# Performance work log

Hardware: AMD Instinct MI355X
Metric: run time of the kernel (lower is better)

Reference implementation:

```python
import jax, jax.numpy as jnp
import numpy as np

B, N, F_DIM = 64, 4096, 64
K_SLOTS, D, N_ITERS = 8, 64, 3
EPS = 1e-8
LN_EPS = 1e-5  # torch LayerNorm default


def layernorm(x, g, b):
    mu = jnp.mean(x, axis=-1, keepdims=True)
    var = jnp.mean(jnp.square(x - mu), axis=-1, keepdims=True)
    return (x - mu) * jax.lax.rsqrt(var + LN_EPS) * g + b


def gru_cell(x, h, w_ih, w_hh, b_ih, b_hh):
    # torch.nn.GRUCell semantics; weights are [3D, D] with gate order r, z, n
    gi = x @ w_ih.T + b_ih
    gh = h @ w_hh.T + b_hh
    i_r, i_z, i_n = jnp.split(gi, 3, axis=-1)
    h_r, h_z, h_n = jnp.split(gh, 3, axis=-1)
    r = jax.nn.sigmoid(i_r + h_r)
    z = jax.nn.sigmoid(i_z + h_z)
    n = jnp.tanh(i_n + r * h_n)
    return (1.0 - z) * n + z * h


def setup_inputs() -> dict:
    key = jax.random.key(0)
    ks = jax.random.split(key, 16)
    f32 = jnp.float32
    s = 0.05  # small init scale for weights
    return {
        "inputs": jax.random.normal(ks[0], (B, N, F_DIM), f32),
        "slots_noise": jax.random.normal(ks[1], (B, K_SLOTS, D), f32),
        "slots_mu": jax.random.normal(ks[2], (1, 1, D), f32) * s,
        "slots_log_sigma": jax.random.normal(ks[3], (1, 1, D), f32) * s,
        "Wq": jax.random.normal(ks[4], (D, D), f32) * s,
        "Wk": jax.random.normal(ks[5], (D, F_DIM), f32) * s,
        "Wv": jax.random.normal(ks[6], (D, F_DIM), f32) * s,
        "gru_w_ih": jax.random.normal(ks[7], (3 * D, D), f32) * s,
        "gru_w_hh": jax.random.normal(ks[8], (3 * D, D), f32) * s,
        "gru_b_ih": jnp.zeros((3 * D,), f32),
        "gru_b_hh": jnp.zeros((3 * D,), f32),
        "mlp_w1": jax.random.normal(ks[9], (2 * D, D), f32) * s,
        "mlp_b1": jnp.zeros((2 * D,), f32),
        "mlp_w2": jax.random.normal(ks[10], (D, 2 * D), f32) * s,
        "mlp_b2": jnp.zeros((D,), f32),
        "ln_in_g": jnp.ones((F_DIM,), f32), "ln_in_b": jnp.zeros((F_DIM,), f32),
        "ln_slots_g": jnp.ones((D,), f32), "ln_slots_b": jnp.zeros((D,), f32),
        "ln_mlp_g": jnp.ones((D,), f32), "ln_mlp_b": jnp.zeros((D,), f32),
    }


def reference(inputs, slots_noise, slots_mu, slots_log_sigma, Wq, Wk, Wv,
              gru_w_ih, gru_w_hh, gru_b_ih, gru_b_hh,
              mlp_w1, mlp_b1, mlp_w2, mlp_b2,
              ln_in_g, ln_in_b, ln_slots_g, ln_slots_b, ln_mlp_g, ln_mlp_b):
    x = layernorm(inputs, ln_in_g, ln_in_b)          # [B, N, F]
    k = jnp.einsum('bnf,df->bnd', x, Wk)             # [B, N, D]
    v = jnp.einsum('bnf,df->bnd', x, Wv)             # [B, N, D]

    slots = slots_mu + jnp.exp(slots_log_sigma) * slots_noise  # [B, K, D]
    scale = D ** -0.5

    for _ in range(N_ITERS):
        slots_prev = slots
        s_n = layernorm(slots, ln_slots_g, ln_slots_b)
        q = jnp.einsum('bkd,ed->bke', s_n, Wq)                  # [B, K, D]
        attn_logits = jnp.einsum('bnd,bkd->bnk', k, q) * scale  # [B, N, K]
        attn = jax.nn.softmax(attn_logits, axis=-1) + EPS       # softmax over slots
        attn = attn / jnp.sum(attn, axis=1, keepdims=True)      # renormalize over N
        updates = jnp.einsum('bnk,bnd->bkd', attn, v)           # [B, K, D]
        slots = gru_cell(updates.reshape(-1, D), slots_prev.reshape(-1, D),
                         gru_w_ih, gru_w_hh, gru_b_ih, gru_b_hh).reshape(B, K_SLOTS, D)
        h = layernorm(slots, ln_mlp_g, ln_mlp_b)
        h = jax.nn.relu(h @ mlp_w1.T + mlp_b1) @ mlp_w2.T + mlp_b2
        slots = slots + h
    return slots
```

## Files before the change

kernel.cpp:

```cpp
#include <hip/hip_runtime.h>
#include <math.h>

#define NN 4096
#define LN_EPS 1e-5f
#define EPS 1e-8f

typedef unsigned short ushortT;
typedef unsigned int uintT;
typedef __attribute__((ext_vector_type(8))) short short8;
typedef __attribute__((ext_vector_type(4))) float f32x4;
typedef __attribute__((ext_vector_type(4))) unsigned short us4;

#define OFF_XN    0L
#define OFF_QT    33554432L
#define OFF_ACC   33587200L
#define OFF_COL   33619968L
#define OFF_SLOTS 33620480L
#define OFF_WIHT  33653248L
#define OFF_WHHT  33665536L
#define OFF_W1T   33677824L
#define OFF_W2T   33686016L
#define OFF_WQT   33694208L
#define OFF_WVT   33698304L
#define OFF_CNT   33702400L

__device__ __forceinline__ float wredsum(float v) {
#pragma unroll
  for (int off = 32; off > 0; off >>= 1) v += __shfl_xor(v, off);
  return v;
}

__device__ __forceinline__ ushortT f2bf(float f) {
  uintT b = __float_as_uint(f);
  b += 0x7fff + ((b >> 16) & 1);
  return (ushortT)(b >> 16);
}

__global__ __launch_bounds__(256) void k_prep(
    const float* __restrict__ w_ih, const float* __restrict__ w_hh,
    const float* __restrict__ w1, const float* __restrict__ w2,
    const float* __restrict__ Wq, const float* __restrict__ Wv,
    float* __restrict__ wihT, float* __restrict__ whhT,
    float* __restrict__ w1T, float* __restrict__ w2T, float* __restrict__ wqT,
    float* __restrict__ wvT, uintT* __restrict__ cnt)
{
  int idx = blockIdx.x * 256 + threadIdx.x;
  if (idx < 12288) {
    int j = idx >> 6, f = idx & 63;
    wihT[f * 192 + j] = w_ih[idx];
  } else if (idx < 24576) {
    int i = idx - 12288; int j = i >> 6, f = i & 63;
    whhT[f * 192 + j] = w_hh[i];
  } else if (idx < 32768) {
    int i = idx - 24576; int j = i >> 6, f = i & 63;
    w1T[f * 128 + j] = w1[i];
  } else if (idx < 40960) {
    int i = idx - 32768; int d = i >> 7, j = i & 127;
    w2T[j * 64 + d] = w2[i];
  } else if (idx < 45056) {
    int i = idx - 40960; int e = i >> 6, d = i & 63;
    wqT[d * 64 + e] = Wq[i];
  } else if (idx < 49152) {
    int i = idx - 45056; int d = i >> 6, f = i & 63;
    wvT[f * 64 + d] = Wv[i];
  } else if (idx < 49216) {
    cnt[idx - 49152] = 0u;
  }
}

__global__ __launch_bounds__(256) void k_ln_init(
    const float* __restrict__ inp,
    const float* __restrict__ g, const float* __restrict__ bbv,
    ushortT* __restrict__ xnG,
    const float* __restrict__ noise, const float* __restrict__ smu,
    const float* __restrict__ slsig, const float* __restrict__ wqT,
    const float* __restrict__ Wk,
    const float* __restrict__ g_sl, const float* __restrict__ b_sl,
    float* __restrict__ slots, ushortT* __restrict__ qF,
    float* __restrict__ acc, float* __restrict__ colsum)
{
  __shared__ __align__(16) ushortT xnF[4096];
  const int tid = threadIdx.x;
  const int lane = tid & 63;
  const int wave = tid >> 6;

  if (blockIdx.x >= 4096) {
    const int bi = blockIdx.x - 4096;
    const int row = bi * 4 + wave;
    const int b = row >> 3, ks = row & 7;
    float* SI = (float*)&xnF[0];
    float* Sw = SI + (wave << 9);

    float s0 = fmaf(expf(slsig[lane]), noise[row * 64 + lane], smu[lane]);
    slots[row * 64 + lane] = s0;
    acc[row * 64 + lane] = 0.f;
    if (lane == 0) colsum[row] = 0.f;

    float mu = wredsum(s0) * (1.f / 64.f);
    float dx = s0 - mu;
    float var = wredsum(dx * dx) * (1.f / 64.f);
    float sn = dx * rsqrtf(var + LN_EPS) * g_sl[lane] + b_sl[lane];
    Sw[lane] = sn;
    float qe = 0.f;
#pragma unroll 16
    for (int d = 0; d < 64; ++d) qe = fmaf(Sw[d], wqT[d * 64 + lane], qe);
    Sw[64 + lane] = qe;
    float qp = 0.f;
#pragma unroll 16
    for (int e = 0; e < 64; ++e) qp = fmaf(Sw[64 + e], Wk[e * 64 + lane], qp);
    const int kb = lane >> 5, lrow = (lane & 31) >> 3, j = lane & 7;
    qF[((((b * 2 + kb) << 6) + (lrow << 4) + ks) << 3) + j] = f2bf(qp * 0.125f);
    qF[((((b * 2 + kb) << 6) + (lrow << 4) + 8 + ks) << 3) + j] = 0;
    return;
  }

  const int l15 = lane & 15, q = lane >> 4;
  const int tile = blockIdx.x;
  const int b = tile >> 6;
  const int c = tile & 63;
  const int n0 = c << 6;
  const float* rowbase = inp + (((long)b * NN + n0) << 6);
  const float4 g4 = *(const float4*)&g[l15 << 2];
  const float4 b4 = *(const float4*)&bbv[l15 << 2];

#pragma unroll
  for (int i = 0; i < 4; ++i) {
    const int row = (wave << 4) + (i << 2) + q;
    float4 x = *(const float4*)&rowbase[(row << 6) + (l15 << 2)];
    float s = x.x + x.y + x.z + x.w;
    s += __shfl_xor(s, 1); s += __shfl_xor(s, 2);
    s += __shfl_xor(s, 4); s += __shfl_xor(s, 8);
    const float mu = s * (1.f / 64.f);
    float4 dx = {x.x - mu, x.y - mu, x.z - mu, x.w - mu};
    float ss = dx.x * dx.x + dx.y * dx.y + dx.z * dx.z + dx.w * dx.w;
    ss += __shfl_xor(ss, 1); ss += __shfl_xor(ss, 2);
    ss += __shfl_xor(ss, 4); ss += __shfl_xor(ss, 8);
    const float rs = rsqrtf(ss * (1.f / 64.f) + LN_EPS);
    us4 p = {f2bf(dx.x * rs * g4.x + b4.x), f2bf(dx.y * rs * g4.y + b4.y),
             f2bf(dx.z * rs * g4.z + b4.z), f2bf(dx.w * rs * g4.w + b4.w)};
    *(us4*)&xnF[((((wave << 1) + (l15 >> 3)) << 6) + (((l15 & 7) >> 1) << 4)
                 + (row & 15)) * 8 + ((l15 & 1) << 2)] = p;
  }
  __syncthreads();

  ushortT* dst = xnG + ((long)(b * 64 + c) << 12);
  short8 v0 = *(const short8*)&xnF[tid << 4];
  short8 v1 = *(const short8*)&xnF[(tid << 4) + 8];
  *(short8*)&dst[tid << 4] = v0;
  *(short8*)&dst[(tid << 4) + 8] = v1;
}

__global__ __launch_bounds__(256, 2) void k_attn(
    const ushortT* __restrict__ xnG,
    ushortT* __restrict__ qF,
    float* __restrict__ acc, float* __restrict__ colsum,
    uintT* __restrict__ cnt, float* __restrict__ slots,
    const float* __restrict__ wihT, const float* __restrict__ whhT,
    const float* __restrict__ w1T, const float* __restrict__ w2T,
    const float* __restrict__ wqT, const float* __restrict__ Wk,
    const float* __restrict__ wvT,
    const float* __restrict__ b_ih, const float* __restrict__ b_hh,
    const float* __restrict__ mb1, const float* __restrict__ mb2,
    const float* __restrict__ g_ml, const float* __restrict__ b_ml,
    const float* __restrict__ g_sl, const float* __restrict__ b_sl,
    float* __restrict__ dout)
{
  __shared__ __align__(16) ushortT XW[4][4096];
  __shared__ int lastFlag;
  const int tid = threadIdx.x;
  const int lane = tid & 63;
  const int wave = tid >> 6;
  const int l15 = lane & 15, q = lane >> 4;
  const int b = blockIdx.x >> 3;
  const int e = blockIdx.x & 7;

  ushortT* xT = &XW[wave][0];

  const ushortT* pc0 = xnG + ((long)(b * 64 + (e << 3) + wave) << 12);
  const ushortT* pc1 = pc0 + (4L << 12);

  short8 kA0[4][2], kA1[4][2];
#pragma unroll
  for (int mt = 0; mt < 4; ++mt)
#pragma unroll
    for (int kb = 0; kb < 2; ++kb) {
      kA0[mt][kb] = *(const short8*)&pc0[((mt * 2 + kb) * 64 + lane) << 3];
      kA1[mt][kb] = *(const short8*)&pc1[((mt * 2 + kb) * 64 + lane) << 3];
    }
  short8 qB[2];
#pragma unroll
  for (int kb = 0; kb < 2; ++kb)
    qB[kb] = *(const short8*)&qF[(((b * 2 + kb) << 6) + lane) << 3];

  f32x4 accP[4];
#pragma unroll
  for (int nt = 0; nt < 4; ++nt) accP[nt] = (f32x4){0.f, 0.f, 0.f, 0.f};
  float csum = 0.f;

  auto do_chunk = [&](const short8 (&kA)[4][2]) {
    f32x4 accL[4];
#pragma unroll
    for (int mt = 0; mt < 4; ++mt) {
      accL[mt] = (f32x4){0.f, 0.f, 0.f, 0.f};
      accL[mt] = __builtin_amdgcn_mfma_f32_16x16x32_bf16(kA[mt][0], qB[0], accL[mt], 0, 0, 0);
      accL[mt] = __builtin_amdgcn_mfma_f32_16x16x32_bf16(kA[mt][1], qB[1], accL[mt], 0, 0, 0);
    }

    {
      const int h = ((lane >> 5) << 2) | (((lane & 15) >> 3) << 1) | ((lane >> 4) & 1);
      const int jp = lane & 7;
      const int lpA = (((lane >> 4) & 1) << 3) + (((lane & 15) >> 3) << 4);
#pragma unroll
      for (int mt = 0; mt < 4; ++mt)
#pragma unroll
        for (int kb = 0; kb < 2; ++kb) {
          const int fb = (kb * 4 + ((lane >> 5) << 1) + (mt >> 1)) << 9;
          const int lm = lpA + ((mt & 1) << 5);
          const ushortT* src = (const ushortT*)&kA[mt][kb];
#pragma unroll
          for (int j = 0; j < 8; ++j)
            xT[fb + (((lm + j) ^ h) << 3) + jp] = src[j];
        }
    }
    short8 vB[4][2];
#pragma unroll
    for (int nt = 0; nt < 4; ++nt)
#pragma unroll
      for (int ks = 0; ks < 2; ++ks) {
        const int frag = nt * 2 + ks;
        const int hr = ((nt & 1) << 2) | (((lane >> 4) & 1) << 1) | ((lane >> 3) & 1);
        vB[nt][ks] = *(const short8*)&xT[(frag << 9) + ((lane ^ hr) << 3)];
      }

    ushortT* attnF = &XW[wave][0];
#pragma unroll
    for (int mt = 0; mt < 4; ++mt) {
      float av[4];
#pragma unroll
      for (int r = 0; r < 4; ++r) {
        float lv = accL[mt][r];
        float mx = lv;
        mx = fmaxf(mx, __shfl_xor(mx, 1));
        mx = fmaxf(mx, __shfl_xor(mx, 2));
        mx = fmaxf(mx, __shfl_xor(mx, 4));
        float ev = __expf(lv - mx);
        float sv = ev;
        sv += __shfl_xor(sv, 1); sv += __shfl_xor(sv, 2); sv += __shfl_xor(sv, 4);
        float a = ev * (1.f / sv) + EPS;
        av[r] = a;
        csum += a;
      }
      us4 p = {f2bf(av[0]), f2bf(av[1]), f2bf(av[2]), f2bf(av[3])};
      *(us4*)&attnF[((((mt >> 1) << 6) + (((mt & 1) * 2 + (q >> 1)) << 4)
                      + l15) << 3) + ((q & 1) << 2)] = p;
    }

    short8 pA0 = *(const short8*)&attnF[(0 * 64 + lane) << 3];
    short8 pA1 = *(const short8*)&attnF[(1 * 64 + lane) << 3];

#pragma unroll
    for (int nt = 0; nt < 4; ++nt) {
      accP[nt] = __builtin_amdgcn_mfma_f32_16x16x32_bf16(pA0, vB[nt][0], accP[nt], 0, 0, 0);
      accP[nt] = __builtin_amdgcn_mfma_f32_16x16x32_bf16(pA1, vB[nt][1], accP[nt], 0, 0, 0);
    }
  };

  do_chunk(kA0);
  do_chunk(kA1);

  csum += __shfl_xor(csum, 16);
  csum += __shfl_xor(csum, 32);

  float* accLw = (float*)&XW[wave][1024];
  float* colLw = (float*)&XW[wave][2048];
  if (q < 2) {
#pragma unroll
    for (int nt = 0; nt < 4; ++nt)
#pragma unroll
      for (int r = 0; r < 4; ++r)
        accLw[(q * 4 + r) * 64 + nt * 16 + l15] = accP[nt][r];
  }
  if (q == 0 && l15 < 8) colLw[l15] = csum;
  __syncthreads();

#pragma unroll
  for (int r = 0; r < 2; ++r) {
    const int o = tid + r * 256;
    const int kk = o >> 6, d = o & 63;
    float s = *((float*)&XW[0][1024] + kk * 64 + d)
            + *((float*)&XW[1][1024] + kk * 64 + d)
            + *((float*)&XW[2][1024] + kk * 64 + d)
            + *((float*)&XW[3][1024] + kk * 64 + d);
    atomicAdd(&acc[(b * 8 + kk) * 64 + d], s);
  }
  if (tid < 8) {
    float s = *((float*)&XW[0][2048] + tid) + *((float*)&XW[1][2048] + tid)
            + *((float*)&XW[2][2048] + tid) + *((float*)&XW[3][2048] + tid);
    atomicAdd(&colsum[b * 8 + tid], s);
  }

  __syncthreads();
  if (tid == 0) lastFlag = (atomicAdd(&cnt[b], 1u) == 7u);
  __syncthreads();
  if (!lastFlag) return;

  const int ks0 = wave, ks1 = wave + 4;
  const int row0 = b * 8 + ks0, row1 = b * 8 + ks1;

  float csv0 = 0.f, csv1 = 0.f;
  if (lane == 0) {
    csv0 = atomicAdd(&colsum[row0], 0.f);
    csv1 = atomicAdd(&colsum[row1], 0.f);
  }
  csv0 = __shfl(csv0, 0); csv1 = __shfl(csv1, 0);
  const float t0 = atomicAdd(&acc[row0 * 64 + lane], 0.f) / csv0;
  const float t1 = atomicAdd(&acc[row1 * 64 + lane], 0.f) / csv1;
  const float h0 = slots[row0 * 64 + lane];
  const float h1 = slots[row1 * 64 + lane];

  float* S = (float*)&XW[wave][0];

  S[256 + lane] = t0; S[320 + lane] = t1;
  float u0 = 0.f, u1 = 0.f;
#pragma unroll 4
  for (int f = 0; f < 64; ++f) {
    const float wv = wvT[f * 64 + lane];
    u0 = fmaf(S[256 + f], wv, u0);
    u1 = fmaf(S[320 + f], wv, u1);
  }

  S[lane] = u0; S[64 + lane] = u1; S[128 + lane] = h0; S[192 + lane] = h1;

  float gir0 = b_ih[lane], giz0 = b_ih[64 + lane], gin0 = b_ih[128 + lane];
  float ghr0 = b_hh[lane], ghz0 = b_hh[64 + lane], ghn0 = b_hh[128 + lane];
  float gir1 = gir0, giz1 = giz0, gin1 = gin0;
  float ghr1 = ghr0, ghz1 = ghz0, ghn1 = ghn0;
#pragma unroll 4
  for (int f = 0; f < 64; ++f) {
    const float wr = wihT[f * 192 + lane], wz = wihT[f * 192 + 64 + lane],
                wn = wihT[f * 192 + 128 + lane];
    const float vr = whhT[f * 192 + lane], vz = whhT[f * 192 + 64 + lane],
                vn = whhT[f * 192 + 128 + lane];
    const float a0 = S[f], a1 = S[64 + f], c0 = S[128 + f], c1 = S[192 + f];
    gir0 = fmaf(a0, wr, gir0); gir1 = fmaf(a1, wr, gir1);
    giz0 = fmaf(a0, wz, giz0); giz1 = fmaf(a1, wz, giz1);
    gin0 = fmaf(a0, wn, gin0); gin1 = fmaf(a1, wn, gin1);
    ghr0 = fmaf(c0, vr, ghr0); ghr1 = fmaf(c1, vr, ghr1);
    ghz0 = fmaf(c0, vz, ghz0); ghz1 = fmaf(c1, vz, ghz1);
    ghn0 = fmaf(c0, vn, ghn0); ghn1 = fmaf(c1, vn, ghn1);
  }
  const float r0 = 1.f / (1.f + expf(-(gir0 + ghr0)));
  const float z0 = 1.f / (1.f + expf(-(giz0 + ghz0)));
  const float n0 = tanhf(fmaf(r0, ghn0, gin0));
  const float hn0 = (1.f - z0) * n0 + z0 * h0;
  const float r1 = 1.f / (1.f + expf(-(gir1 + ghr1)));
  const float z1 = 1.f / (1.f + expf(-(giz1 + ghz1)));
  const float n1 = tanhf(fmaf(r1, ghn1, gin1));
  const float hn1 = (1.f - z1) * n1 + z1 * h1;

  float mu0 = wredsum(hn0) * (1.f / 64.f);
  float dx0 = hn0 - mu0;
  float va0 = wredsum(dx0 * dx0) * (1.f / 64.f);
  const float ln0 = dx0 * rsqrtf(va0 + LN_EPS) * g_ml[lane] + b_ml[lane];
  float mu1 = wredsum(hn1) * (1.f / 64.f);
  float dx1 = hn1 - mu1;
  float va1 = wredsum(dx1 * dx1) * (1.f / 64.f);
  const float ln1 = dx1 * rsqrtf(va1 + LN_EPS) * g_ml[lane] + b_ml[lane];
  S[256 + lane] = ln0; S[320 + lane] = ln1;

  float h1a0 = mb1[lane], h1b0 = mb1[64 + lane];
  float h1a1 = h1a0, h1b1 = h1b0;
#pragma unroll 4
  for (int f = 0; f < 64; ++f) {
    const float wa = w1T[f * 128 + lane], wb = w1T[f * 128 + 64 + lane];
    const float l0 = S[256 + f], l1 = S[320 + f];
    h1a0 = fmaf(l0, wa, h1a0); h1a1 = fmaf(l1, wa, h1a1);
    h1b0 = fmaf(l0, wb, h1b0); h1b1 = fmaf(l1, wb, h1b1);
  }
  h1a0 = fmaxf(h1a0, 0.f); h1b0 = fmaxf(h1b0, 0.f);
  h1a1 = fmaxf(h1a1, 0.f); h1b1 = fmaxf(h1b1, 0.f);
  S[lane] = h1a0; S[64 + lane] = h1b0;
  S[128 + lane] = h1a1; S[192 + lane] = h1b1;

  float o0 = mb2[lane], o1 = mb2[lane];
#pragma unroll 4
  for (int j = 0; j < 128; ++j) {
    const float w2v = w2T[j * 64 + lane];
    o0 = fmaf(S[j], w2v, o0);
    o1 = fmaf(S[128 + j], w2v, o1);
  }
  const float sn0 = hn0 + o0;
  const float sn1 = hn1 + o1;
  slots[row0 * 64 + lane] = sn0;
  slots[row1 * 64 + lane] = sn1;
  if (dout) {
    dout[row0 * 64 + lane] = sn0;
    dout[row1 * 64 + lane] = sn1;
  }

  float m20 = wredsum(sn0) * (1.f / 64.f);
  float d20 = sn0 - m20;
  float v20 = wredsum(d20 * d20) * (1.f / 64.f);
  const float sq0 = d20 * rsqrtf(v20 + LN_EPS) * g_sl[lane] + b_sl[lane];
  float m21 = wredsum(sn1) * (1.f / 64.f);
  float d21 = sn1 - m21;
  float v21 = wredsum(d21 * d21) * (1.f / 64.f);
  const float sq1 = d21 * rsqrtf(v21 + LN_EPS) * g_sl[lane] + b_sl[lane];
  S[256 + lane] = sq0; S[320 + lane] = sq1;
  float qe0 = 0.f, qe1 = 0.f;
#pragma unroll 8
  for (int d = 0; d < 64; ++d) {
    const float wq = wqT[d * 64 + lane];
    qe0 = fmaf(S[256 + d], wq, qe0);
    qe1 = fmaf(S[320 + d], wq, qe1);
  }
  S[384 + lane] = qe0; S[448 + lane] = qe1;
  float qp0 = 0.f, qp1 = 0.f;
#pragma unroll 8
  for (int e2 = 0; e2 < 64; ++e2) {
    const float wk = Wk[e2 * 64 + lane];
    qp0 = fmaf(S[384 + e2], wk, qp0);
    qp1 = fmaf(S[448 + e2], wk, qp1);
  }
  const int kb = lane >> 5, lrow = (lane & 31) >> 3, jj = lane & 7;
  qF[((((b * 2 + kb) << 6) + (lrow << 4) + ks0) << 3) + jj] = f2bf(qp0 * 0.125f);
  qF[((((b * 2 + kb) << 6) + (lrow << 4) + ks1) << 3) + jj] = f2bf(qp1 * 0.125f);

  acc[row0 * 64 + lane] = 0.f;
  acc[row1 * 64 + lane] = 0.f;
  if (lane == 0) { colsum[row0] = 0.f; colsum[row1] = 0.f; }
  if (tid == 0) cnt[b] = 0u;
}

extern "C" void kernel_launch(void* const* d_in, const int* in_sizes, int n_in,
                              void* d_out, int out_size, void* d_ws, size_t ws_size,
                              hipStream_t stream) {
  const float* inp   = (const float*)d_in[0];
  const float* noise = (const float*)d_in[1];
  const float* smu   = (const float*)d_in[2];
  const float* slsig = (const float*)d_in[3];
  const float* Wq    = (const float*)d_in[4];
  const float* Wk    = (const float*)d_in[5];
  const float* Wv    = (const float*)d_in[6];
  const float* w_ih  = (const float*)d_in[7];
  const float* w_hh  = (const float*)d_in[8];
  const float* b_ih  = (const float*)d_in[9];
  const float* b_hh  = (const float*)d_in[10];
  const float* w1    = (const float*)d_in[11];
  const float* b1    = (const float*)d_in[12];
  const float* w2    = (const float*)d_in[13];
  const float* b2    = (const float*)d_in[14];
  const float* g_in  = (const float*)d_in[15];
  const float* bi_in = (const float*)d_in[16];
  const float* g_sl  = (const float*)d_in[17];
  const float* bi_sl = (const float*)d_in[18];
  const float* g_ml  = (const float*)d_in[19];
  const float* bi_ml = (const float*)d_in[20];

  float* ws      = (float*)d_ws;
  ushortT* xnG   = (ushortT*)(ws + OFF_XN);
  ushortT* qF    = (ushortT*)(ws + OFF_QT);
  float* ac      = ws + OFF_ACC;
  float* cs      = ws + OFF_COL;
  float* sl      = ws + OFF_SLOTS;
  float* wihT    = ws + OFF_WIHT;
  float* whhT    = ws + OFF_WHHT;
  float* w1T     = ws + OFF_W1T;
  float* w2T     = ws + OFF_W2T;
  float* wqT     = ws + OFF_WQT;
  float* wvT     = ws + OFF_WVT;
  uintT* cnt     = (uintT*)(ws + OFF_CNT);

  k_prep<<<193, 256, 0, stream>>>(w_ih, w_hh, w1, w2, Wq, Wv,
                                  wihT, whhT, w1T, w2T, wqT, wvT, cnt);
  k_ln_init<<<4224, 256, 0, stream>>>(inp, g_in, bi_in, xnG,
                                      noise, smu, slsig, wqT, Wk, g_sl, bi_sl,
                                      sl, qF, ac, cs);
  for (int it = 0; it < 3; ++it) {
    k_attn<<<512, 256, 0, stream>>>(xnG, qF, ac, cs, cnt, sl,
                                    wihT, whhT, w1T, w2T, wqT, Wk, wvT,
                                    b_ih, b_hh, b1, b2, g_ml, bi_ml, g_sl, bi_sl,
                                    it == 2 ? (float*)d_out : nullptr);
  }
}
```

Before: 255.7 us.

## Fuse three attention iterations into one persistent kernel with per-batch ready flags

Replaces the three k_attn launches with a single launch. Each block keeps its bf16 K/V fragments in registers across all iterations and spin-waits on a per-batch ready counter that the last-arriving block bumps after it writes the new queries. The accumulators and counters are triple-buffered per iteration so nothing has to be reset between rounds, and the query handoff now goes through packed uint atomics. This removes two kernel launches and the repeated reload of the normalized inputs. It depends on all 512 blocks being co-resident (two per CU); if they are not, the spin-wait can deadlock.

```diff
diff --git a/kernel.cpp b/kernel.cpp
--- a/kernel.cpp
+++ b/kernel.cpp
@@ -12,17 +12,18 @@
 typedef __attribute__((ext_vector_type(4))) unsigned short us4;
 
 #define OFF_XN    0L
-#define OFF_QT    33554432L
-#define OFF_ACC   33587200L
-#define OFF_COL   33619968L
-#define OFF_SLOTS 33620480L
-#define OFF_WIHT  33653248L
-#define OFF_WHHT  33665536L
-#define OFF_W1T   33677824L
-#define OFF_W2T   33686016L
-#define OFF_WQT   33694208L
-#define OFF_WVT   33698304L
-#define OFF_CNT   33702400L
+#define OFF_QU    8388608L
+#define OFF_ACC   8421376L
+#define OFF_COL   8519680L
+#define OFF_SLOTS 8521216L
+#define OFF_WIHT  8553984L
+#define OFF_WHHT  8566272L
+#define OFF_W1T   8578560L
+#define OFF_W2T   8586752L
+#define OFF_WQT   8594944L
+#define OFF_WVT   8599040L
+#define OFF_CNT   8603136L
+#define OFF_RDY   8603328L
 
 __device__ __forceinline__ float wredsum(float v) {
 #pragma unroll
@@ -34,6 +35,10 @@
   uintT b = __float_as_uint(f);
   b += 0x7fff + ((b >> 16) & 1);
   return (ushortT)(b >> 16);
+}
+
+__device__ __forceinline__ uintT pack2bf(float lo, float hi) {
+  return (uintT)f2bf(lo) | ((uintT)f2bf(hi) << 16);
 }
 
 __global__ __launch_bounds__(256) void k_prep(
@@ -42,7 +47,7 @@
     const float* __restrict__ Wq, const float* __restrict__ Wv,
     float* __restrict__ wihT, float* __restrict__ whhT,
     float* __restrict__ w1T, float* __restrict__ w2T, float* __restrict__ wqT,
-    float* __restrict__ wvT, uintT* __restrict__ cnt)
+    float* __restrict__ wvT, uintT* __restrict__ cnt, uintT* __restrict__ ready)
 {
   int idx = blockIdx.x * 256 + threadIdx.x;
   if (idx < 12288) {
@@ -63,8 +68,10 @@
   } else if (idx < 49152) {
     int i = idx - 45056; int d = i >> 6, f = i & 63;
     wvT[f * 64 + d] = Wv[i];
-  } else if (idx < 49216) {
+  } else if (idx < 49344) {
     cnt[idx - 49152] = 0u;
+  } else if (idx < 49408) {
+    ready[idx - 49344] = 0u;
   }
 }
 
@@ -76,7 +83,7 @@
     const float* __restrict__ slsig, const float* __restrict__ wqT,
     const float* __restrict__ Wk,
     const float* __restrict__ g_sl, const float* __restrict__ b_sl,
-    float* __restrict__ slots, ushortT* __restrict__ qF,
+    float* __restrict__ slots, uintT* __restrict__ qU,
     float* __restrict__ acc, float* __restrict__ colsum)
 {
   __shared__ __align__(16) ushortT xnF[4096];
@@ -93,8 +100,11 @@
 
     float s0 = fmaf(expf(slsig[lane]), noise[row * 64 + lane], smu[lane]);
     slots[row * 64 + lane] = s0;
-    acc[row * 64 + lane] = 0.f;
-    if (lane == 0) colsum[row] = 0.f;
+#pragma unroll
+    for (int it = 0; it < 3; ++it) {
+      acc[it * 32768 + row * 64 + lane] = 0.f;
+      if (lane == 0) colsum[it * 512 + row] = 0.f;
+    }
 
     float mu = wredsum(s0) * (1.f / 64.f);
     float dx = s0 - mu;
@@ -108,9 +118,14 @@
     float qp = 0.f;
 #pragma unroll 16
     for (int e = 0; e < 64; ++e) qp = fmaf(Sw[64 + e], Wk[e * 64 + lane], qp);
-    const int kb = lane >> 5, lrow = (lane & 31) >> 3, j = lane & 7;
-    qF[((((b * 2 + kb) << 6) + (lrow << 4) + ks) << 3) + j] = f2bf(qp * 0.125f);
-    qF[((((b * 2 + kb) << 6) + (lrow << 4) + 8 + ks) << 3) + j] = 0;
+    Sw[128 + lane] = qp * 0.125f;
+    if (lane < 32) {
+      const int kb = lane >> 4, lrow = (lane >> 2) & 3, j2 = lane & 3;
+      const int fA = kb * 32 + lrow * 8 + 2 * j2;
+      uintT u = pack2bf(Sw[128 + fA], Sw[128 + fA + 1]);
+      qU[((b * 2 + kb) * 64 + lrow * 16 + ks) * 4 + j2] = u;
+      qU[((b * 2 + kb) * 64 + lrow * 16 + 8 + ks) * 4 + j2] = 0u;
+    }
     return;
   }
 
@@ -151,10 +166,10 @@
 }
 
 __global__ __launch_bounds__(256, 2) void k_attn(
-    const ushortT* __restrict__ xnG,
-    ushortT* __restrict__ qF,
+    const ushortT* __restrict__ xnG, uintT* __restrict__ qU,
     float* __restrict__ acc, float* __restrict__ colsum,
-    uintT* __restrict__ cnt, float* __restrict__ slots,
+    uintT* __restrict__ cnt, uintT* __restrict__ ready,
+    float* __restrict__ slots,
     const float* __restrict__ wihT, const float* __restrict__ whhT,
     const float* __restrict__ w1T, const float* __restrict__ w2T,
     const float* __restrict__ wqT, const float* __restrict__ Wk,
@@ -187,249 +202,274 @@
       kA0[mt][kb] = *(const short8*)&pc0[((mt * 2 + kb) * 64 + lane) << 3];
       kA1[mt][kb] = *(const short8*)&pc1[((mt * 2 + kb) * 64 + lane) << 3];
     }
-  short8 qB[2];
-#pragma unroll
-  for (int kb = 0; kb < 2; ++kb)
-    qB[kb] = *(const short8*)&qF[(((b * 2 + kb) << 6) + lane) << 3];
-
-  f32x4 accP[4];
-#pragma unroll
-  for (int nt = 0; nt < 4; ++nt) accP[nt] = (f32x4){0.f, 0.f, 0.f, 0.f};
-  float csum = 0.f;
-
-  auto do_chunk = [&](const short8 (&kA)[4][2]) {
-    f32x4 accL[4];
-#pragma unroll
-    for (int mt = 0; mt < 4; ++mt) {
-      accL[mt] = (f32x4){0.f, 0.f, 0.f, 0.f};
-      accL[mt] = __builtin_amdgcn_mfma_f32_16x16x32_bf16(kA[mt][0], qB[0], accL[mt], 0, 0, 0);
-      accL[mt] = __builtin_amdgcn_mfma_f32_16x16x32_bf16(kA[mt][1], qB[1], accL[mt], 0, 0, 0);
-    }
-
-    {
-      const int h = ((lane >> 5) << 2) | (((lane & 15) >> 3) << 1) | ((lane >> 4) & 1);
-      const int jp = lane & 7;
-      const int lpA = (((lane >> 4) & 1) << 3) + (((lane & 15) >> 3) << 4);
-#pragma unroll
-      for (int mt = 0; mt < 4; ++mt)
-#pragma unroll
-        for (int kb = 0; kb < 2; ++kb) {
-          const int fb = (kb * 4 + ((lane >> 5) << 1) + (mt >> 1)) << 9;
-          const int lm = lpA + ((mt & 1) << 5);
-          const ushortT* src = (const ushortT*)&kA[mt][kb];
-#pragma unroll
-          for (int j = 0; j < 8; ++j)
-            xT[fb + (((lm + j) ^ h) << 3) + jp] = src[j];
+
+  for (int it = 0; it < 3; ++it) {
+    if (it > 0) {
+      if (tid == 0) {
+        while (atomicAdd(&ready[b], 0u) < (uintT)it) __builtin_amdgcn_s_sleep(2);
+      }
+      __syncthreads();
+    }
+
+    short8 qB[2];
+#pragma unroll
+    for (int kb = 0; kb < 2; ++kb) {
+      uintT uu[4];
+#pragma unroll
+      for (int j2 = 0; j2 < 4; ++j2)
+        uu[j2] = atomicAdd(&qU[((b * 2 + kb) * 64 + lane) * 4 + j2], 0u);
+      qB[kb] = *(short8*)uu;
+    }
+
+    f32x4 accP[4];
+#pragma unroll
+    for (int nt = 0; nt < 4; ++nt) accP[nt] = (f32x4){0.f, 0.f, 0.f, 0.f};
+    float csum = 0.f;
+
+#pragma unroll
+    for (int ch = 0; ch < 2; ++ch) {
+      f32x4 accL[4];
+#pragma unroll
+      for (int mt = 0; mt < 4; ++mt) {
+        const short8 a0 = ch ? kA1[mt][0] : kA0[mt][0];
+        const short8 a1 = ch ? kA1[mt][1] : kA0[mt][1];
+        accL[mt] = (f32x4){0.f, 0.f, 0.f, 0.f};
+        accL[mt] = __builtin_amdgcn_mfma_f32_16x16x32_bf16(a0, qB[0], accL[mt], 0, 0, 0);
+        accL[mt] = __builtin_amdgcn_mfma_f32_16x16x32_bf16(a1, qB[1], accL[mt], 0, 0, 0);
+      }
+
+      {
+        const int h = ((lane >> 5) << 2) | (((lane & 15) >> 3) << 1) | ((lane >> 4) & 1);
+        const int jp = lane & 7;
+        const int lpA = (((lane >> 4) & 1) << 3) + (((lane & 15) >> 3) << 4);
+#pragma unroll
+        for (int mt = 0; mt < 4; ++mt)
+#pragma unroll
+          for (int kb = 0; kb < 2; ++kb) {
+            const int fb = (kb * 4 + ((lane >> 5) << 1) + (mt >> 1)) << 9;
+            const int lm = lpA + ((mt & 1) << 5);
+            const short8 src8 = ch ? kA1[mt][kb] : kA0[mt][kb];
+            const ushortT* src = (const ushortT*)&src8;
+#pragma unroll
+            for (int j = 0; j < 8; ++j)
+              xT[fb + (((lm + j) ^ h) << 3) + jp] = src[j];
+          }
+      }
+      short8 vB[4][2];
+#pragma unroll
+      for (int nt = 0; nt < 4; ++nt)
+#pragma unroll
+        for (int ks = 0; ks < 2; ++ks) {
+          const int frag = nt * 2 + ks;
+          const int hr = ((nt & 1) << 2) | (((lane >> 4) & 1) << 1) | ((lane >> 3) & 1);
+          vB[nt][ks] = *(const short8*)&xT[(frag << 9) + ((lane ^ hr) << 3)];
         }
-    }
-    short8 vB[4][2];
-#pragma unroll
-    for (int nt = 0; nt < 4; ++nt)
-#pragma unroll
-      for (int ks = 0; ks < 2; ++ks) {
-        const int frag = nt * 2 + ks;
-        const int hr = ((nt & 1) << 2) | (((lane >> 4) & 1) << 1) | ((lane >> 3) & 1);
-        vB[nt][ks] = *(const short8*)&xT[(frag << 9) + ((lane ^ hr) << 3)];
-      }
-
-    ushortT* attnF = &XW[wave][0];
-#pragma unroll
-    for (int mt = 0; mt < 4; ++mt) {
-      float av[4];
-#pragma unroll
-      for (int r = 0; r < 4; ++r) {
-        float lv = accL[mt][r];
-        float mx = lv;
-        mx = fmaxf(mx, __shfl_xor(mx, 1));
-        mx = fmaxf(mx, __shfl_xor(mx, 2));
-        mx = fmaxf(mx, __shfl_xor(mx, 4));
-        float ev = __expf(lv - mx);
-        float sv = ev;
-        sv += __shfl_xor(sv, 1); sv += __shfl_xor(sv, 2); sv += __shfl_xor(sv, 4);
-        float a = ev * (1.f / sv) + EPS;
-        av[r] = a;
-        csum += a;
-      }
-      us4 p = {f2bf(av[0]), f2bf(av[1]), f2bf(av[2]), f2bf(av[3])};
-      *(us4*)&attnF[((((mt >> 1) << 6) + (((mt & 1) * 2 + (q >> 1)) << 4)
-                      + l15) << 3) + ((q & 1) << 2)] = p;
-    }
-
-    short8 pA0 = *(const short8*)&attnF[(0 * 64 + lane) << 3];
-    short8 pA1 = *(const short8*)&attnF[(1 * 64 + lane) << 3];
-
-#pragma unroll
-    for (int nt = 0; nt < 4; ++nt) {
-      accP[nt] = __builtin_amdgcn_mfma_f32_16x16x32_bf16(pA0, vB[nt][0], accP[nt], 0, 0, 0);
-      accP[nt] = __builtin_amdgcn_mfma_f32_16x16x32_bf16(pA1, vB[nt][1], accP[nt], 0, 0, 0);
-    }
-  };
-
-  do_chunk(kA0);
-  do_chunk(kA1);
-
-  csum += __shfl_xor(csum, 16);
-  csum += __shfl_xor(csum, 32);
-
-  float* accLw = (float*)&XW[wave][1024];
-  float* colLw = (float*)&XW[wave][2048];
-  if (q < 2) {
-#pragma unroll
-    for (int nt = 0; nt < 4; ++nt)
-#pragma unroll
-      for (int r = 0; r < 4; ++r)
-        accLw[(q * 4 + r) * 64 + nt * 16 + l15] = accP[nt][r];
+
+      ushortT* attnF = &XW[wave][0];
+#pragma unroll
+      for (int mt = 0; mt < 4; ++mt) {
+        float av[4];
+#pragma unroll
+        for (int r = 0; r < 4; ++r) {
+          float lv = accL[mt][r];
+          float mx = lv;
+          mx = fmaxf(mx, __shfl_xor(mx, 1));
+          mx = fmaxf(mx, __shfl_xor(mx, 2));
+          mx = fmaxf(mx, __shfl_xor(mx, 4));
+          float ev = __expf(lv - mx);
+          float sv = ev;
+          sv += __shfl_xor(sv, 1); sv += __shfl_xor(sv, 2); sv += __shfl_xor(sv, 4);
+          float a = ev * (1.f / sv) + EPS;
+          av[r] = a;
+          csum += a;
+        }
+        us4 p = {f2bf(av[0]), f2bf(av[1]), f2bf(av[2]), f2bf(av[3])};
+        *(us4*)&attnF[((((mt >> 1) << 6) + (((mt & 1) * 2 + (q >> 1)) << 4)
+                        + l15) << 3) + ((q & 1) << 2)] = p;
+      }
+
+      short8 pA0 = *(const short8*)&attnF[(0 * 64 + lane) << 3];
+      short8 pA1 = *(const short8*)&attnF[(1 * 64 + lane) << 3];
+
+#pragma unroll
+      for (int nt = 0; nt < 4; ++nt) {
+        accP[nt] = __builtin_amdgcn_mfma_f32_16x16x32_bf16(pA0, vB[nt][0], accP[nt], 0, 0, 0);
+        accP[nt] = __builtin_amdgcn_mfma_f32_16x16x32_bf16(pA1, vB[nt][1], accP[nt], 0, 0, 0);
+      }
+    }
+
+    csum += __shfl_xor(csum, 16);
+    csum += __shfl_xor(csum, 32);
+
+    float* accLw = (float*)&XW[wave][1024];
+    float* colLw = (float*)&XW[wave][2048];
+    if (q < 2) {
+#pragma unroll
+      for (int nt = 0; nt < 4; ++nt)
+#pragma unroll
+        for (int r = 0; r < 4; ++r)
+          accLw[(q * 4 + r) * 64 + nt * 16 + l15] = accP[nt][r];
+    }
+    if (q == 0 && l15 < 8) colLw[l15] = csum;
+    __syncthreads();
+
+    float* accIt = acc + it * 32768;
+    float* colIt = colsum + it * 512;
+#pragma unroll
+    for (int r = 0; r < 2; ++r) {
+      const int o = tid + r * 256;
+      const int kk = o >> 6, d = o & 63;
+      float s = *((float*)&XW[0][1024] + kk * 64 + d)
+              + *((float*)&XW[1][1024] + kk * 64 + d)
+              + *((float*)&XW[2][1024] + kk * 64 + d)
+              + *((float*)&XW[3][1024] + kk * 64 + d);
+      atomicAdd(&accIt[(b * 8 + kk) * 64 + d], s);
+    }
+    if (tid < 8) {
+      float s = *((float*)&XW[0][2048] + tid) + *((float*)&XW[1][2048] + tid)
+              + *((float*)&XW[2][2048] + tid) + *((float*)&XW[3][2048] + tid);
+      atomicAdd(&colIt[b * 8 + tid], s);
+    }
+
+    __syncthreads();
+    if (tid == 0) lastFlag = (atomicAdd(&cnt[it * 64 + b], 1u) == 7u);
+    __syncthreads();
+
+    if (lastFlag) {
+      const int ks0 = wave, ks1 = wave + 4;
+      const int row0 = b * 8 + ks0, row1 = b * 8 + ks1;
+
+      float csv0 = 0.f, csv1 = 0.f;
+      if (lane == 0) {
+        csv0 = atomicAdd(&colIt[row0], 0.f);
+        csv1 = atomicAdd(&colIt[row1], 0.f);
+      }
+      csv0 = __shfl(csv0, 0); csv1 = __shfl(csv1, 0);
+      const float t0 = atomicAdd(&accIt[row0 * 64 + lane], 0.f) / csv0;
+      const float t1 = atomicAdd(&accIt[row1 * 64 + lane], 0.f) / csv1;
+      const float h0 = atomicAdd(&slots[row0 * 64 + lane], 0.f);
+      const float h1 = atomicAdd(&slots[row1 * 64 + lane], 0.f);
+
+      float* S = (float*)&XW[wave][0];
+
+      S[256 + lane] = t0; S[320 + lane] = t1;
+      float u0 = 0.f, u1 = 0.f;
+#pragma unroll 4
+      for (int f = 0; f < 64; ++f) {
+        const float wv = wvT[f * 64 + lane];
+        u0 = fmaf(S[256 + f], wv, u0);
+        u1 = fmaf(S[320 + f], wv, u1);
+      }
+
+      S[lane] = u0; S[64 + lane] = u1; S[128 + lane] = h0; S[192 + lane] = h1;
+
+      float gir0 = b_ih[lane], giz0 = b_ih[64 + lane], gin0 = b_ih[128 + lane];
+      float ghr0 = b_hh[lane], ghz0 = b_hh[64 + lane], ghn0 = b_hh[128 + lane];
+      float gir1 = gir0, giz1 = giz0, gin1 = gin0;
+      float ghr1 = ghr0, ghz1 = ghz0, ghn1 = ghn0;
+#pragma unroll 4
+      for (int f = 0; f < 64; ++f) {
+        const float wr = wihT[f * 192 + lane], wz = wihT[f * 192 + 64 + lane],
+                    wn = wihT[f * 192 + 128 + lane];
+        const float vr = whhT[f * 192 + lane], vz = whhT[f * 192 + 64 + lane],
+                    vn = whhT[f * 192 + 128 + lane];
+        const float a0 = S[f], a1 = S[64 + f], c0 = S[128 + f], c1 = S[192 + f];
+        gir0 = fmaf(a0, wr, gir0); gir1 = fmaf(a1, wr, gir1);
+        giz0 = fmaf(a0, wz, giz0); giz1 = fmaf(a1, wz, giz1);
+        gin0 = fmaf(a0, wn, gin0); gin1 = fmaf(a1, wn, gin1);
+        ghr0 = fmaf(c0, vr, ghr0); ghr1 = fmaf(c1, vr, ghr1);
+        ghz0 = fmaf(c0, vz, ghz0); ghz1 = fmaf(c1, vz, ghz1);
+        ghn0 = fmaf(c0, vn, ghn0); ghn1 = fmaf(c1, vn, ghn1);
+      }
+      const float r0 = 1.f / (1.f + expf(-(gir0 + ghr0)));
+      const float z0 = 1.f / (1.f + expf(-(giz0 + ghz0)));
+      const float n0 = tanhf(fmaf(r0, ghn0, gin0));
+      const float hn0 = (1.f - z0) * n0 + z0 * h0;
+      const float r1 = 1.f / (1.f + expf(-(gir1 + ghr1)));
+      const float z1 = 1.f / (1.f + expf(-(giz1 + ghz1)));
+      const float n1 = tanhf(fmaf(r1, ghn1, gin1));
+      const float hn1 = (1.f - z1) * n1 + z1 * h1;
+
+      float mu0 = wredsum(hn0) * (1.f / 64.f);
+      float dx0 = hn0 - mu0;
+      float va0 = wredsum(dx0 * dx0) * (1.f / 64.f);
+      const float ln0 = dx0 * rsqrtf(va0 + LN_EPS) * g_ml[lane] + b_ml[lane];
+      float mu1 = wredsum(hn1) * (1.f / 64.f);
+      float dx1 = hn1 - mu1;
+      float va1 = wredsum(dx1 * dx1) * (1.f / 64.f);
+      const float ln1 = dx1 * rsqrtf(va1 + LN_EPS) * g_ml[lane] + b_ml[lane];
+      S[256 + lane] = ln0; S[320 + lane] = ln1;
+
+      float h1a0 = mb1[lane], h1b0 = mb1[64 + lane];
+      float h1a1 = h1a0, h1b1 = h1b0;
+#pragma unroll 4
+      for (int f = 0; f < 64; ++f) {
+        const float wa = w1T[f * 128 + lane], wb = w1T[f * 128 + 64 + lane];
+        const float l0 = S[256 + f], l1 = S[320 + f];
+        h1a0 = fmaf(l0, wa, h1a0); h1a1 = fmaf(l1, wa, h1a1);
+        h1b0 = fmaf(l0, wb, h1b0); h1b1 = fmaf(l1, wb, h1b1);
+      }
+      h1a0 = fmaxf(h1a0, 0.f); h1b0 = fmaxf(h1b0, 0.f);
+      h1a1 = fmaxf(h1a1, 0.f); h1b1 = fmaxf(h1b1, 0.f);
+      S[lane] = h1a0; S[64 + lane] = h1b0;
+      S[128 + lane] = h1a1; S[192 + lane] = h1b1;
+
+      float o0 = mb2[lane], o1 = mb2[lane];
+#pragma unroll 4
+      for (int j = 0; j < 128; ++j) {
+        const float w2v = w2T[j * 64 + lane];
+        o0 = fmaf(S[j], w2v, o0);
+        o1 = fmaf(S[128 + j], w2v, o1);
+      }
+      const float sn0 = hn0 + o0;
+      const float sn1 = hn1 + o1;
+
+      if (it == 2) {
+        dout[row0 * 64 + lane] = sn0;
+        dout[row1 * 64 + lane] = sn1;
+      } else {
+        atomicExch(&slots[row0 * 64 + lane], sn0);
+        atomicExch(&slots[row1 * 64 + lane], sn1);
+
+        float m20 = wredsum(sn0) * (1.f / 64.f);
+        float d20 = sn0 - m20;
+        float v20 = wredsum(d20 * d20) * (1.f / 64.f);
+        const float sq0 = d20 * rsqrtf(v20 + LN_EPS) * g_sl[lane] + b_sl[lane];
+        float m21 = wredsum(sn1) * (1.f / 64.f);
+        float d21 = sn1 - m21;
+        float v21 = wredsum(d21 * d21) * (1.f / 64.f);
+        const float sq1 = d21 * rsqrtf(v21 + LN_EPS) * g_sl[lane] + b_sl[lane];
+        S[256 + lane] = sq0; S[320 + lane] = sq1;
+        float qe0 = 0.f, qe1 = 0.f;
+#pragma unroll 8
+        for (int d = 0; d < 64; ++d) {
+          const float wq = wqT[d * 64 + lane];
+          qe0 = fmaf(S[256 + d], wq, qe0);
+          qe1 = fmaf(S[320 + d], wq, qe1);
+        }
+        S[256 + lane] = qe0; S[320 + lane] = qe1;
+        float qp0 = 0.f, qp1 = 0.f;
+#pragma unroll 8
+        for (int e2 = 0; e2 < 64; ++e2) {
+          const float wk = Wk[e2 * 64 + lane];
+          qp0 = fmaf(S[256 + e2], wk, qp0);
+          qp1 = fmaf(S[320 + e2], wk, qp1);
+        }
+        S[384 + lane] = qp0 * 0.125f;
+        S[448 + lane] = qp1 * 0.125f;
+        {
+          const int rr = lane >> 5, L5 = lane & 31;
+          const int kb = L5 >> 4, lrow = (L5 >> 2) & 3, j2 = L5 & 3;
+          const int fA = kb * 32 + lrow * 8 + 2 * j2;
+          const int ksr = rr ? ks1 : ks0;
+          uintT u = pack2bf(S[384 + rr * 64 + fA], S[384 + rr * 64 + fA + 1]);
+          atomicExch(&qU[((b * 2 + kb) * 64 + lrow * 16 + ksr) * 4 + j2], u);
+        }
+        __syncthreads();
+        if (tid == 0) atomicAdd(&ready[b], 1u);
+      }
+    }
   }
-  if (q == 0 && l15 < 8) colLw[l15] = csum;
-  __syncthreads();
-
-#pragma unroll
-  for (int r = 0; r < 2; ++r) {
-    const int o = tid + r * 256;
-    const int kk = o >> 6, d = o & 63;
-    float s = *((float*)&XW[0][1024] + kk * 64 + d)
-            + *((float*)&XW[1][1024] + kk * 64 + d)
-            + *((float*)&XW[2][1024] + kk * 64 + d)
-            + *((float*)&XW[3][1024] + kk * 64 + d);
-    atomicAdd(&acc[(b * 8 + kk) * 64 + d], s);
-  }
-  if (tid < 8) {
-    float s = *((float*)&XW[0][2048] + tid) + *((float*)&XW[1][2048] + tid)
-            + *((float*)&XW[2][2048] + tid) + *((float*)&XW[3][2048] + tid);
-    atomicAdd(&colsum[b * 8 + tid], s);
-  }
-
-  __syncthreads();
-  if (tid == 0) lastFlag = (atomicAdd(&cnt[b], 1u) == 7u);
-  __syncthreads();
-  if (!lastFlag) return;
-
-  const int ks0 = wave, ks1 = wave + 4;
-  const int row0 = b * 8 + ks0, row1 = b * 8 + ks1;
-
-  float csv0 = 0.f, csv1 = 0.f;
-  if (lane == 0) {
-    csv0 = atomicAdd(&colsum[row0], 0.f);
-    csv1 = atomicAdd(&colsum[row1], 0.f);
-  }
-  csv0 = __shfl(csv0, 0); csv1 = __shfl(csv1, 0);
-  const float t0 = atomicAdd(&acc[row0 * 64 + lane], 0.f) / csv0;
-  const float t1 = atomicAdd(&acc[row1 * 64 + lane], 0.f) / csv1;
-  const float h0 = slots[row0 * 64 + lane];
-  const float h1 = slots[row1 * 64 + lane];
-
-  float* S = (float*)&XW[wave][0];
-
-  S[256 + lane] = t0; S[320 + lane] = t1;
-  float u0 = 0.f, u1 = 0.f;
-#pragma unroll 4
-  for (int f = 0; f < 64; ++f) {
-    const float wv = wvT[f * 64 + lane];
-    u0 = fmaf(S[256 + f], wv, u0);
-    u1 = fmaf(S[320 + f], wv, u1);
-  }
-
-  S[lane] = u0; S[64 + lane] = u1; S[128 + lane] = h0; S[192 + lane] = h1;
-
-  float gir0 = b_ih[lane], giz0 = b_ih[64 + lane], gin0 = b_ih[128 + lane];
-  float ghr0 = b_hh[lane], ghz0 = b_hh[64 + lane], ghn0 = b_hh[128 + lane];
-  float gir1 = gir0, giz1 = giz0, gin1 = gin0;
-  float ghr1 = ghr0, ghz1 = ghz0, ghn1 = ghn0;
-#pragma unroll 4
-  for (int f = 0; f < 64; ++f) {
-    const float wr = wihT[f * 192 + lane], wz = wihT[f * 192 + 64 + lane],
-                wn = wihT[f * 192 + 128 + lane];
-    const float vr = whhT[f * 192 + lane], vz = whhT[f * 192 + 64 + lane],
-                vn = whhT[f * 192 + 128 + lane];
-    const float a0 = S[f], a1 = S[64 + f], c0 = S[128 + f], c1 = S[192 + f];
-    gir0 = fmaf(a0, wr, gir0); gir1 = fmaf(a1, wr, gir1);
-    giz0 = fmaf(a0, wz, giz0); giz1 = fmaf(a1, wz, giz1);
-    gin0 = fmaf(a0, wn, gin0); gin1 = fmaf(a1, wn, gin1);
-    ghr0 = fmaf(c0, vr, ghr0); ghr1 = fmaf(c1, vr, ghr1);
-    ghz0 = fmaf(c0, vz, ghz0); ghz1 = fmaf(c1, vz, ghz1);
-    ghn0 = fmaf(c0, vn, ghn0); ghn1 = fmaf(c1, vn, ghn1);
-  }
-  const float r0 = 1.f / (1.f + expf(-(gir0 + ghr0)));
-  const float z0 = 1.f / (1.f + expf(-(giz0 + ghz0)));
-  const float n0 = tanhf(fmaf(r0, ghn0, gin0));
-  const float hn0 = (1.f - z0) * n0 + z0 * h0;
-  const float r1 = 1.f / (1.f + expf(-(gir1 + ghr1)));
-  const float z1 = 1.f / (1.f + expf(-(giz1 + ghz1)));
-  const float n1 = tanhf(fmaf(r1, ghn1, gin1));
-  const float hn1 = (1.f - z1) * n1 + z1 * h1;
-
-  float mu0 = wredsum(hn0) * (1.f / 64.f);
-  float dx0 = hn0 - mu0;
-  float va0 = wredsum(dx0 * dx0) * (1.f / 64.f);
-  const float ln0 = dx0 * rsqrtf(va0 + LN_EPS) * g_ml[lane] + b_ml[lane];
-  float mu1 = wredsum(hn1) * (1.f / 64.f);
-  float dx1 = hn1 - mu1;
-  float va1 = wredsum(dx1 * dx1) * (1.f / 64.f);
-  const float ln1 = dx1 * rsqrtf(va1 + LN_EPS) * g_ml[lane] + b_ml[lane];
-  S[256 + lane] = ln0; S[320 + lane] = ln1;
-
-  float h1a0 = mb1[lane], h1b0 = mb1[64 + lane];
-  float h1a1 = h1a0, h1b1 = h1b0;
-#pragma unroll 4
-  for (int f = 0; f < 64; ++f) {
-    const float wa = w1T[f * 128 + lane], wb = w1T[f * 128 + 64 + lane];
-    const float l0 = S[256 + f], l1 = S[320 + f];
-    h1a0 = fmaf(l0, wa, h1a0); h1a1 = fmaf(l1, wa, h1a1);
-    h1b0 = fmaf(l0, wb, h1b0); h1b1 = fmaf(l1, wb, h1b1);
-  }
-  h1a0 = fmaxf(h1a0, 0.f); h1b0 = fmaxf(h1b0, 0.f);
-  h1a1 = fmaxf(h1a1, 0.f); h1b1 = fmaxf(h1b1, 0.f);
-  S[lane] = h1a0; S[64 + lane] = h1b0;
-  S[128 + lane] = h1a1; S[192 + lane] = h1b1;
-
-  float o0 = mb2[lane], o1 = mb2[lane];
-#pragma unroll 4
-  for (int j = 0; j < 128; ++j) {
-    const float w2v = w2T[j * 64 + lane];
-    o0 = fmaf(S[j], w2v, o0);
-    o1 = fmaf(S[128 + j], w2v, o1);
-  }
-  const float sn0 = hn0 + o0;
-  const float sn1 = hn1 + o1;
-  slots[row0 * 64 + lane] = sn0;
-  slots[row1 * 64 + lane] = sn1;
-  if (dout) {
-    dout[row0 * 64 + lane] = sn0;
-    dout[row1 * 64 + lane] = sn1;
-  }
-
-  float m20 = wredsum(sn0) * (1.f / 64.f);
-  float d20 = sn0 - m20;
-  float v20 = wredsum(d20 * d20) * (1.f / 64.f);
-  const float sq0 = d20 * rsqrtf(v20 + LN_EPS) * g_sl[lane] + b_sl[lane];
-  float m21 = wredsum(sn1) * (1.f / 64.f);
-  float d21 = sn1 - m21;
-  float v21 = wredsum(d21 * d21) * (1.f / 64.f);
-  const float sq1 = d21 * rsqrtf(v21 + LN_EPS) * g_sl[lane] + b_sl[lane];
-  S[256 + lane] = sq0; S[320 + lane] = sq1;
-  float qe0 = 0.f, qe1 = 0.f;
-#pragma unroll 8
-  for (int d = 0; d < 64; ++d) {
-    const float wq = wqT[d * 64 + lane];
-    qe0 = fmaf(S[256 + d], wq, qe0);
-    qe1 = fmaf(S[320 + d], wq, qe1);
-  }
-  S[384 + lane] = qe0; S[448 + lane] = qe1;
-  float qp0 = 0.f, qp1 = 0.f;
-#pragma unroll 8
-  for (int e2 = 0; e2 < 64; ++e2) {
-    const float wk = Wk[e2 * 64 + lane];
-    qp0 = fmaf(S[384 + e2], wk, qp0);
-    qp1 = fmaf(S[448 + e2], wk, qp1);
-  }
-  const int kb = lane >> 5, lrow = (lane & 31) >> 3, jj = lane & 7;
-  qF[((((b * 2 + kb) << 6) + (lrow << 4) + ks0) << 3) + jj] = f2bf(qp0 * 0.125f);
-  qF[((((b * 2 + kb) << 6) + (lrow << 4) + ks1) << 3) + jj] = f2bf(qp1 * 0.125f);
-
-  acc[row0 * 64 + lane] = 0.f;
-  acc[row1 * 64 + lane] = 0.f;
-  if (lane == 0) { colsum[row0] = 0.f; colsum[row1] = 0.f; }
-  if (tid == 0) cnt[b] = 0u;
 }
 
 extern "C" void kernel_launch(void* const* d_in, const int* in_sizes, int n_in,
@@ -459,7 +499,7 @@
 
   float* ws      = (float*)d_ws;
   ushortT* xnG   = (ushortT*)(ws + OFF_XN);
-  ushortT* qF    = (ushortT*)(ws + OFF_QT);
+  uintT* qU      = (uintT*)(ws + OFF_QU);
   float* ac      = ws + OFF_ACC;
   float* cs      = ws + OFF_COL;
   float* sl      = ws + OFF_SLOTS;
@@ -470,16 +510,15 @@
   float* wqT     = ws + OFF_WQT;
   float* wvT     = ws + OFF_WVT;
   uintT* cnt     = (uintT*)(ws + OFF_CNT);
-
-  k_prep<<<193, 256, 0, stream>>>(w_ih, w_hh, w1, w2, Wq, Wv,
-                                  wihT, whhT, w1T, w2T, wqT, wvT, cnt);
+  uintT* rdy     = (uintT*)(ws + OFF_RDY);
+
+  k_prep<<<194, 256, 0, stream>>>(w_ih, w_hh, w1, w2, Wq, Wv,
+                                  wihT, whhT, w1T, w2T, wqT, wvT, cnt, rdy);
   k_ln_init<<<4224, 256, 0, stream>>>(inp, g_in, bi_in, xnG,
                                       noise, smu, slsig, wqT, Wk, g_sl, bi_sl,
-                                      sl, qF, ac, cs);
-  for (int it = 0; it < 3; ++it) {
-    k_attn<<<512, 256, 0, stream>>>(xnG, qF, ac, cs, cnt, sl,
-                                    wihT, whhT, w1T, w2T, wqT, Wk, wvT,
-                                    b_ih, b_hh, b1, b2, g_ml, bi_ml, g_sl, bi_sl,
-                                    it == 2 ? (float*)d_out : nullptr);
-  }
-}
+                                      sl, qU, ac, cs);
+  k_attn<<<512, 256, 0, stream>>>(xnG, qU, ac, cs, cnt, rdy, sl,
+                                  wihT, whhT, w1T, w2T, wqT, Wk, wvT,
+                                  b_ih, b_hh, b1, b2, g_ml, bi_ml, g_sl, bi_sl,
+                                  (float*)d_out);
+}
```

Result: no change. 259.7 us (+1.6%).
